# Kernel tuning notes

Hardware: AMD Instinct MI355X
Metric: run time of the kernel (lower is better)

Reference implementation:

```python
import jax, jax.numpy as jnp
import numpy as np

B, N, K = 8, 2048, 20
NC = 50
EPS = 1e-5
SLOPE = 0.2


def _knn(xt, k):
    # xt: [B, N, C]; negative squared euclidean distance, top-k (includes self)
    xx = jnp.sum(xt * xt, axis=-1)                      # [B, N]
    inner = jnp.einsum('bnc,bmc->bnm', xt, xt)          # [B, N, N]
    dist = 2.0 * inner - xx[:, :, None] - xx[:, None, :]
    return jax.lax.top_k(dist, k)[1]                    # [B, N, k] int32


def _edge_conv(xt, w, g, b, k):
    # xt: [B, N, C]; w: [O, 2C]; BatchNorm2d over (B, N, k) per out-channel.
    idx = _knn(xt, k)
    nbr = xt[jnp.arange(B)[:, None, None], idx]          # [B, N, k, C]
    ctr = jnp.broadcast_to(xt[:, :, None, :], nbr.shape)
    edge = jnp.concatenate([nbr - ctr, ctr], axis=-1)    # [B, N, k, 2C]
    h = jnp.einsum('bnkc,oc->bnko', edge, w)             # 1x1 conv, no bias
    mu = jnp.mean(h, axis=(0, 1, 2))
    var = jnp.var(h, axis=(0, 1, 2))
    h = (h - mu) / jnp.sqrt(var + EPS) * g + b
    h = jnp.where(h > 0, h, SLOPE * h)                   # LeakyReLU(0.2)
    return jnp.max(h, axis=2)                            # max over k -> [B, N, O]


def _bn1d(y, g, b):
    mu = jnp.mean(y, axis=0)
    var = jnp.var(y, axis=0)
    return (y - mu) / jnp.sqrt(var + EPS) * g + b


def setup_inputs() -> dict:
    key = jax.random.key(0)
    ks = jax.random.split(key, 20)

    def rn(k, shape, scale):
        return jax.random.normal(k, shape, dtype=jnp.float32) * scale

    d = {
        'x': rn(ks[0], (B * N, 3), 1.0),
        'pos': rn(ks[1], (B * N, 3), 1.0),
        'batch': jnp.repeat(jnp.arange(B, dtype=jnp.int64), N),
        'edge_index': jax.random.randint(ks[2], (2, B * N), 0, B * N, dtype=jnp.int64),
        # EdgeConv 1x1 conv weights [out, in], BN gamma/beta
        'w1': rn(ks[3], (64, 6), 0.3),   'g1': jnp.ones(64),  'b1': jnp.zeros(64),
        'w2': rn(ks[4], (64, 128), 0.1), 'g2': jnp.ones(64),  'b2': jnp.zeros(64),
        'w3': rn(ks[5], (128, 128), 0.1),'g3': jnp.ones(128), 'b3': jnp.zeros(128),
        'w4': rn(ks[6], (256, 256), 0.08),'g4': jnp.ones(256),'b4': jnp.zeros(256),
        # lin1: Linear(512,1024)+ReLU+BN1d(1024)
        'lw1': rn(ks[7], (512, 1024), 0.04), 'lb1': jnp.zeros(1024),
        'lg1': jnp.ones(1024), 'lbb1': jnp.zeros(1024),
        # mlp: [1024->256 +ReLU+BN] -> [256->128 +ReLU+BN] -> Lin(128, NC)
        'mw1': rn(ks[8], (1024, 256), 0.03), 'mb1': jnp.zeros(256),
        'mg1': jnp.ones(256), 'mbb1': jnp.zeros(256),
        'mw2': rn(ks[9], (256, 128), 0.06), 'mb2': jnp.zeros(128),
        'mg2': jnp.ones(128), 'mbb2': jnp.zeros(128),
        'hw': rn(ks[10], (128, NC), 0.09), 'hb': jnp.zeros(NC),
    }
    return d


def reference(x, pos, batch, edge_index,
              w1, g1, b1, w2, g2, b2, w3, g3, b3, w4, g4, b4,
              lw1, lb1, lg1, lbb1,
              mw1, mb1, mg1, mbb1, mw2, mb2, mg2, mbb2,
              hw, hb):
    # batch is sorted with N points per cloud -> static reshape
    xt = x.reshape(B, N, 3)
    x1 = _edge_conv(xt, w1, g1, b1, K)   # [B, N, 64]
    x2 = _edge_conv(x1, w2, g2, b2, K)   # [B, N, 64]
    x3 = _edge_conv(x2, w3, g3, b3, K)   # [B, N, 128]
    x4 = _edge_conv(x3, w4, g4, b4, K)   # [B, N, 256]
    cat = jnp.concatenate([x1, x2, x3, x4], axis=-1)  # [B, N, 512]
    h = cat.reshape(B * N, 512)
    h = _bn1d(jax.nn.relu(h @ lw1 + lb1), lg1, lbb1)
    h = _bn1d(jax.nn.relu(h @ mw1 + mb1), mg1, mbb1)   # dropout = identity (eval)
    h = _bn1d(jax.nn.relu(h @ mw2 + mb2), mg2, mbb2)
    logits = h @ hw + hb
    return jax.nn.log_softmax(logits, axis=1)
```

## Files before the change

### kernel.cpp

```cpp
#include <hip/hip_runtime.h>
#include <math.h>

#define NB 8
#define NP 2048
#define KNBR 20
#define NROWS (NB*NP)
#define SLOPEV 0.2f
#define EPSV 1e-5f

typedef short s8v __attribute__((ext_vector_type(8)));
typedef float f4v __attribute__((ext_vector_type(4)));
typedef double d4v __attribute__((ext_vector_type(4)));

__device__ __forceinline__ unsigned short f2bf(float f) {
    union { float f; unsigned u; } v; v.f = f;
    unsigned r = v.u + 0x7FFFu + ((v.u >> 16) & 1u);
    return (unsigned short)(r >> 16);
}

__global__ void mfma64_probe(int* __restrict__ tab)
{
    const int lane = threadIdx.x;
    d4v z = {0.0, 0.0, 0.0, 0.0};
    d4v pa = __builtin_amdgcn_mfma_f64_16x16x4f64((double)lane, 1.0, z, 0, 0, 0);
    d4v pb = __builtin_amdgcn_mfma_f64_16x16x4f64(1.0, (double)lane, z, 0, 0, 0);
    int famA = 1, famB = 1;
#pragma unroll
    for (int r = 0; r < 4; ++r) {
        int iv = (int)(pa[r] + 0.5);
        int row;
        if ((iv & 3) == 0 && iv >= 96) row = (iv - 96) >> 2;
        else { row = (iv - 6) >> 4; famA = 0; }
        int jv = (int)(pb[r] + 0.5);
        int col;
        if ((jv & 3) == 0 && jv >= 96) col = (jv - 96) >> 2;
        else { col = (jv - 6) >> 4; famB = 0; }
        tab[lane * 8 + r]     = row;
        tab[lane * 8 + 4 + r] = col;
    }
    tab[512 + lane] = famA;
    tab[576 + lane] = famB;
}

template<int KD>
__global__ __launch_bounds__(256, 2) void knn_fused2(
    const double* __restrict__ F, int lda, int C,
    const double* __restrict__ xx,
    double* __restrict__ tmpv, int* __restrict__ tmpc,
    const int* __restrict__ tab)
{
    constexpr int CH = (KD < 16) ? KD : 16;
    __shared__ double Bs[CH][66];
    __shared__ double Tile[64][65];
    __shared__ double thr[64];
    __shared__ unsigned msk[64][2];

    const int tid = threadIdx.x;
    const int wave = tid >> 6, lane = tid & 63;
    const int bb    = blockIdx.z;
    const int half  = blockIdx.y;
    const int r0    = blockIdx.x * 64;
    const int cbase = half * 1024;
    const double* Fb  = F  + (size_t)bb * NP * lda;
    const double* xxb = xx + (size_t)bb * NP;

    int rT[4], cT[4];
#pragma unroll
    for (int r = 0; r < 4; ++r) { rT[r] = tab[lane * 8 + r]; cT[r] = tab[lane * 8 + 4 + r]; }
    const int famA = tab[512];
    const int famB = tab[576];
    const int am = famA ? (lane & 15) : (lane >> 2);
    const int ak = famA ? (lane >> 4) : (lane & 3);
    const int bn = famB ? (lane & 15) : (lane >> 2);
    const int bk = famB ? (lane >> 4) : (lane & 3);

    const int arow = r0 + wave * 16 + am;
    double areg[KD / 4];
#pragma unroll
    for (int j = 0; j < KD / 4; ++j) {
        const int k = j * 4 + ak;
        areg[j] = (k < C) ? Fb[(size_t)arow * lda + k] : 0.0;
    }
    double xr4[4];
#pragma unroll
    for (int rg = 0; rg < 4; ++rg)
        xr4[rg] = xxb[r0 + wave * 16 + rT[rg]];

    double kv[KNBR];
    int    ki[KNBR];
#pragma unroll
    for (int q = 0; q < KNBR; ++q) { kv[q] = -INFINITY; ki[q] = 0; }
    if (tid < 64) { thr[tid] = -INFINITY; msk[tid][0] = 0u; msk[tid][1] = 0u; }
    __syncthreads();

    for (int ct = 0; ct < 16; ++ct) {
        const int c0 = cbase + ct * 64;
        d4v acc[4];
#pragma unroll
        for (int nt = 0; nt < 4; ++nt) acc[nt] = (d4v){0.0, 0.0, 0.0, 0.0};

#pragma unroll
        for (int kc = 0; kc < KD; kc += CH) {
            {
                const int col = tid >> 2;
                const int kb0 = (tid & 3) * (CH / 4);
                const double* bp = Fb + (size_t)(c0 + col) * lda + kc + kb0;
#pragma unroll
                for (int i = 0; i < CH / 4; ++i) {
                    const int k2 = kc + kb0 + i;
                    Bs[kb0 + i][col] = (k2 < C) ? bp[i] : 0.0;
                }
            }
            __syncthreads();
#pragma unroll
            for (int kg = 0; kg < CH / 4; ++kg) {
                const double a  = areg[kc / 4 + kg];
                const double b0 = Bs[kg * 4 + bk][bn];
                const double b1 = Bs[kg * 4 + bk][16 + bn];
                const double b2 = Bs[kg * 4 + bk][32 + bn];
                const double b3 = Bs[kg * 4 + bk][48 + bn];
                acc[0] = __builtin_amdgcn_mfma_f64_16x16x4f64(a, b0, acc[0], 0, 0, 0);
                acc[1] = __builtin_amdgcn_mfma_f64_16x16x4f64(a, b1, acc[1], 0, 0, 0);
                acc[2] = __builtin_amdgcn_mfma_f64_16x16x4f64(a, b2, acc[2], 0, 0, 0);
                acc[3] = __builtin_amdgcn_mfma_f64_16x16x4f64(a, b3, acc[3], 0, 0, 0);
            }
            __syncthreads();
        }

#pragma unroll
        for (int nt = 0; nt < 4; ++nt) {
#pragma unroll
            for (int rg = 0; rg < 4; ++rg) {
                const int rloc = wave * 16 + rT[rg];
                const int cloc = nt * 16 + cT[rg];
                const double d = (2.0 * acc[nt][rg] - xr4[rg]) - xxb[c0 + cloc];
                if (d > thr[rloc]) {
                    Tile[rloc][cloc] = d;
                    atomicOr(&msk[rloc][cloc >> 5], 1u << (cloc & 31));
                }
            }
        }
        __syncthreads();

        if (tid < 64) {
            bool changed = false;
#pragma unroll
            for (int w2 = 0; w2 < 2; ++w2) {
                unsigned m = msk[tid][w2];
                msk[tid][w2] = 0u;
                while (m) {
                    const int b = __ffs(m) - 1;
                    m &= m - 1u;
                    const double v = Tile[tid][w2 * 32 + b];
                    if (v > kv[KNBR - 1]) {
                        const int col = c0 + w2 * 32 + b;
                        int pos = 0;
#pragma unroll
                        for (int q = 0; q < KNBR; ++q) pos += (kv[q] >= v) ? 1 : 0;
#pragma unroll
                        for (int q = KNBR - 1; q >= 0; --q) {
                            if (q > pos)       { kv[q] = kv[q - 1]; ki[q] = ki[q - 1]; }
                            else if (q == pos) { kv[q] = v;         ki[q] = col; }
                        }
                        changed = true;
                    }
                }
            }
            if (changed) thr[tid] = kv[KNBR - 1];
        }
        __syncthreads();
    }

    if (tid < 64) {
        const size_t rowg = (size_t)bb * NP + r0 + tid;
        double* vp = tmpv + (rowg * 2 + half) * KNBR;
        int*    cp = tmpc + (rowg * 2 + half) * KNBR;
#pragma unroll
        for (int q = 0; q < KNBR; ++q) { vp[q] = kv[q]; cp[q] = ki[q]; }
    }
}

__global__ void merge_topk(const double* __restrict__ tmpv,
                           const int* __restrict__ tmpc,
                           int* __restrict__ out)
{
    const int row = blockIdx.x * 256 + threadIdx.x;
    if (row >= NROWS) return;
    const double* va = tmpv + (size_t)row * 2 * KNBR;
    const int*    ca = tmpc + (size_t)row * 2 * KNBR;
    const double* vb = va + KNBR;
    const int*    cb = ca + KNBR;
    const int jbase = (row / NP) * NP;
    int* op = out + (size_t)row * KNBR;
    int ia = 0, ib = 0;
#pragma unroll
    for (int q = 0; q < KNBR; ++q) {
        const double x = va[ia], y = vb[ib];
        const bool takeA = (x > y) || (x == y && ca[ia] < cb[ib]);
        if (takeA) { op[q] = jbase + ca[ia]; ++ia; }
        else       { op[q] = jbase + cb[ib]; ++ib; }
    }
}

#define DK 16
__global__ __launch_bounds__(256, 2) void gemm64(
    const double* __restrict__ A, int lda,
    const double* __restrict__ Bm, int ldb,
    double* __restrict__ P, double* __restrict__ Q, int O, int Kd,
    const int* __restrict__ tab)
{
    __shared__ double As[DK][130];
    __shared__ double Bs[DK][66];
    const int tid = threadIdx.x;
    const int wave = tid >> 6, lane = tid & 63;
    const int quad = lane >> 4, l15 = lane & 15;
    const int row0 = blockIdx.y * 128, col0 = blockIdx.x * 64;

    int rT[4], cT[4];
#pragma unroll
    for (int r = 0; r < 4; ++r) { rT[r] = tab[lane * 8 + r]; cT[r] = tab[lane * 8 + 4 + r]; }
    const int famA = tab[512];
    const int famB = tab[576];
    const int am = famA ? l15 : (lane >> 2);
    const int ak = famA ? quad : (lane & 3);
    const int bn = famB ? l15 : (lane >> 2);
    const int bk = famB ? quad : (lane & 3);

    d4v acc[2][4];
#pragma unroll
    for (int mt = 0; mt < 2; ++mt)
#pragma unroll
        for (int nt = 0; nt < 4; ++nt) acc[mt][nt] = (d4v){0.0, 0.0, 0.0, 0.0};

    const int ma = tid >> 1, ka = (tid & 1) * 8;
    const int mb = tid >> 2, kb = (tid & 3) * 4;

    for (int kc = 0; kc < Kd; kc += DK) {
        const double* ap = A + (size_t)(row0 + ma) * lda + kc + ka;
#pragma unroll
        for (int i = 0; i < 8; ++i) {
            const int k2 = kc + ka + i;
            As[ka + i][ma] = (k2 < Kd) ? ap[i] : 0.0;
        }
        const double* bp = Bm + (size_t)(col0 + mb) * ldb + kc + kb;
#pragma unroll
        for (int i = 0; i < 4; ++i) {
            const int k2 = kc + kb + i;
            Bs[kb + i][mb] = (k2 < Kd) ? bp[i] : 0.0;
        }
        __syncthreads();
#pragma unroll
        for (int kg = 0; kg < 4; ++kg) {
            const int k = kg * 4;
            double a0 = As[k + ak][wave * 32 + am];
            double a1 = As[k + ak][wave * 32 + 16 + am];
            double b0 = Bs[k + bk][bn];
            double b1 = Bs[k + bk][16 + bn];
            double b2 = Bs[k + bk][32 + bn];
            double b3 = Bs[k + bk][48 + bn];
            acc[0][0] = __builtin_amdgcn_mfma_f64_16x16x4f64(a0, b0, acc[0][0], 0, 0, 0);
            acc[0][1] = __builtin_amdgcn_mfma_f64_16x16x4f64(a0, b1, acc[0][1], 0, 0, 0);
            acc[0][2] = __builtin_amdgcn_mfma_f64_16x16x4f64(a0, b2, acc[0][2], 0, 0, 0);
            acc[0][3] = __builtin_amdgcn_mfma_f64_16x16x4f64(a0, b3, acc[0][3], 0, 0, 0);
            acc[1][0] = __builtin_amdgcn_mfma_f64_16x16x4f64(a1, b0, acc[1][0], 0, 0, 0);
            acc[1][1] = __builtin_amdgcn_mfma_f64_16x16x4f64(a1, b1, acc[1][1], 0, 0, 0);
            acc[1][2] = __builtin_amdgcn_mfma_f64_16x16x4f64(a1, b2, acc[1][2], 0, 0, 0);
            acc[1][3] = __builtin_amdgcn_mfma_f64_16x16x4f64(a1, b3, acc[1][3], 0, 0, 0);
        }
        __syncthreads();
    }

    double* dst = (col0 < O) ? P : Q;
    const int cbase = (col0 < O) ? col0 : (col0 - O);
#pragma unroll
    for (int mt = 0; mt < 2; ++mt)
#pragma unroll
        for (int nt = 0; nt < 4; ++nt) {
#pragma unroll
            for (int rg = 0; rg < 4; ++rg) {
                const int r = row0 + wave * 32 + mt * 16 + rT[rg];
                const int c = cbase + nt * 16 + cT[rg];
                dst[(size_t)r * O + c] = acc[mt][nt][rg];
            }
        }
}

__global__ __launch_bounds__(256) void gemm_bf16(
    const float* __restrict__ A, int lda,
    const unsigned short* __restrict__ W,
    float* __restrict__ C, int ldc,
    int Kd,
    const float* __restrict__ bias,
    const float* __restrict__ a_ss)
{
    __shared__ unsigned short As[4][64][8];
    __shared__ unsigned short Bs[4][128][8];
    const int tid = threadIdx.x;
    const int wave = tid >> 6, lane = tid & 63;
    const int quad = lane >> 4, l15 = lane & 15;
    const int row0 = blockIdx.y * 64, col0 = blockIdx.x * 128;

    f4v acc[4][2];
#pragma unroll
    for (int mt = 0; mt < 4; ++mt)
#pragma unroll
        for (int nt = 0; nt < 2; ++nt) acc[mt][nt] = (f4v){0.f, 0.f, 0.f, 0.f};

    const int ar = tid >> 2, akc = tid & 3;
    const int br = tid >> 1, bkc = (tid & 1) * 2;

    for (int kc0 = 0; kc0 < Kd; kc0 += 32) {
        {
            const float* ap = A + (size_t)(row0 + ar) * lda + kc0 + akc * 8;
            float t0[8];
            *(float4*)&t0[0] = *(const float4*)ap;
            *(float4*)&t0[4] = *(const float4*)(ap + 4);
            if (a_ss) {
                const int kb = kc0 + akc * 8;
#pragma unroll
                for (int i = 0; i < 8; ++i)
                    t0[i] = fmaf(t0[i], a_ss[kb + i], a_ss[Kd + kb + i]);
            }
            unsigned short u[8];
#pragma unroll
            for (int i = 0; i < 8; ++i) u[i] = f2bf(t0[i]);
            *(uint4*)&As[akc][ar][0] = *(const uint4*)&u[0];
        }
        {
            const unsigned short* wp = W + (size_t)(col0 + br) * Kd + kc0 + bkc * 8;
            uint4 q0 = *(const uint4*)wp;
            uint4 q1 = *(const uint4*)(wp + 8);
            *(uint4*)&Bs[bkc][br][0]     = q0;
            *(uint4*)&Bs[bkc + 1][br][0] = q1;
        }
        __syncthreads();

        s8v a[4], b[2];
#pragma unroll
        for (int mt = 0; mt < 4; ++mt)
            a[mt] = *(const s8v*)&As[quad][mt * 16 + l15][0];
#pragma unroll
        for (int nt = 0; nt < 2; ++nt)
            b[nt] = *(const s8v*)&Bs[quad][wave * 32 + nt * 16 + l15][0];
#pragma unroll
        for (int mt = 0; mt < 4; ++mt)
#pragma unroll
            for (int nt = 0; nt < 2; ++nt)
                acc[mt][nt] = __builtin_amdgcn_mfma_f32_16x16x32_bf16(
                    a[mt], b[nt], acc[mt][nt], 0, 0, 0);
        __syncthreads();
    }

#pragma unroll
    for (int mt = 0; mt < 4; ++mt)
#pragma unroll
        for (int nt = 0; nt < 2; ++nt) {
            const int col = col0 + wave * 32 + nt * 16 + l15;
            const float bi = bias[col];
#pragma unroll
            for (int r = 0; r < 4; ++r) {
                const int row = row0 + mt * 16 + quad * 4 + r;
                float v = acc[mt][nt][r] + bi;
                v = fmaxf(v, 0.f);
                C[(size_t)row * ldc + col] = v;
            }
        }
}

#define GBK 16
__global__ __launch_bounds__(256, 2) void gemm_f32(
    const float* __restrict__ A, int lda,
    const float* __restrict__ Bm, int ldb,
    float* __restrict__ Cm, int ldc,
    int M, int Nn, int Kd, int mode,
    const float* __restrict__ bias,
    const float* __restrict__ a_ss)
{
    __shared__ float As[GBK][132];
    __shared__ float Bs[GBK][132];
    const int tid = threadIdx.x;
    const int tx = tid & 15, ty = tid >> 4;
    const int lin = blockIdx.y * gridDim.x + blockIdx.x;
    const int bx = lin / gridDim.y;
    const int by = lin - bx * gridDim.y;
    const int row0 = by * 128, col0 = bx * 128;
    float acc[8][8];
#pragma unroll
    for (int i = 0; i < 8; ++i)
#pragma unroll
        for (int j = 0; j < 8; ++j) acc[i][j] = 0.f;

    const int m  = tid >> 1;
    const int kk = (tid & 1) * 8;

    for (int kc = 0; kc < Kd; kc += GBK) {
        const int gc = col0 + m;
        const float* ap = A  + (size_t)(row0 + m) * lda + kc + kk;
        const float* bp = Bm + (size_t)gc * ldb + kc + kk;
#pragma unroll
        for (int i = 0; i < 8; ++i) {
            const int k2 = kc + kk + i;
            float v = 0.f;
            if (k2 < Kd) {
                v = ap[i];
                if (a_ss) v = fmaf(v, a_ss[k2], a_ss[Kd + k2]);
            }
            As[kk + i][m] = v;
        }
#pragma unroll
        for (int i = 0; i < 8; ++i) {
            const int k2 = kc + kk + i;
            float v = 0.f;
            if (gc < Nn && k2 < Kd) v = bp[i];
            Bs[kk + i][m] = v;
        }
        __syncthreads();
#pragma unroll
        for (int k = 0; k < GBK; ++k) {
            float4 a0 = *(const float4*)&As[k][ty * 4];
            float4 a1 = *(const float4*)&As[k][64 + ty * 4];
            float4 b0 = *(const float4*)&Bs[k][tx * 4];
            float4 b1 = *(const float4*)&Bs[k][64 + tx * 4];
            float a[8] = {a0.x, a0.y, a0.z, a0.w, a1.x, a1.y, a1.z, a1.w};
            float b[8] = {b0.x, b0.y, b0.z, b0.w, b1.x, b1.y, b1.z, b1.w};
#pragma unroll
            for (int i = 0; i < 8; ++i)
#pragma unroll
                for (int j = 0; j < 8; ++j) acc[i][j] = fmaf(a[i], b[j], acc[i][j]);
        }
        __syncthreads();
    }

#pragma unroll
    for (int i = 0; i < 8; ++i) {
        const int row = row0 + ty * 4 + (i & 3) + ((i >> 2) << 6);
        if (row >= M) continue;
#pragma unroll
        for (int h = 0; h < 2; ++h) {
            const int c0 = col0 + tx * 4 + (h << 6);
#pragma unroll
            for (int j = 0; j < 4; ++j) {
                const int col = c0 + j;
                if (col < Nn) {
                    float t = acc[i][h * 4 + j];
                    if (mode == 2)      t = fmaxf(t + bias[col], 0.f);
                    else if (mode == 3) t = t + bias[col];
                    Cm[(size_t)row * ldc + col] = t;
                }
            }
        }
    }
}

__global__ void f2d_kernel(const float* __restrict__ in, double* __restrict__ out, long n)
{
    long t = (long)blockIdx.x * 256 + threadIdx.x;
    if (t < n) out[t] = (double)in[t];
}
__global__ void d2f_kernel(const double* __restrict__ in, float* __restrict__ out, long n)
{
    long t = (long)blockIdx.x * 256 + threadIdx.x;
    if (t < n) out[t] = (float)in[t];
}

__global__ void xx_kernel_d(const double* __restrict__ F, int lda, int C,
                            double* __restrict__ xx)
{
    int r = blockIdx.x * 256 + threadIdx.x;
    if (r >= NROWS) return;
    const double* p = F + (long)r * lda;
    double s = 0.0;
    for (int c = 0; c < C; ++c) { double v = p[c]; s = fma(v, v, s); }
    xx[r] = s;
}

__global__ void wmod_kernel_d(const float* __restrict__ w, double* __restrict__ wm,
                              int O, int C)
{
    int t = blockIdx.x * 256 + threadIdx.x;
    if (t >= O * C) return;
    int o = t / C, c = t - o * C;
    double a = (double)w[o * 2 * C + c];
    double b = (double)w[o * 2 * C + C + c];
    wm[o * C + c] = a;
    wm[(O + o) * C + c] = b - a;
}

__global__ void transpose_kernel(const float* __restrict__ in, float* __restrict__ out,
                                 int R, int C)
{
    long t = (long)blockIdx.x * 256 + threadIdx.x;
    if (t >= (long)R * C) return;
    int r = (int)(t / C), c = (int)(t - (long)r * C);
    out[(long)c * R + r] = in[t];
}

__global__ void transpose_bf(const float* __restrict__ in, unsigned short* __restrict__ out,
                             int R, int C)
{
    long t = (long)blockIdx.x * 256 + threadIdx.x;
    if (t >= (long)R * C) return;
    int r = (int)(t / C), c = (int)(t - (long)r * C);
    out[(long)c * R + r] = f2bf(in[t]);
}

__global__ __launch_bounds__(256) void edge_gather(const double* __restrict__ P,
                                                   const double* __restrict__ Q,
                                                   const int* __restrict__ idx,
                                                   int O, int shiftO,
                                                   double* __restrict__ sums,
                                                   double* __restrict__ catOut, int ldo)
{
    const int tid = threadIdx.x;
    const int o = tid & (O - 1);
    const int q = tid >> shiftO;
    const int nsub = 256 >> shiftO;
    const int lin = blockIdx.x;
    const int r0 = (lin & 7) * NP + (lin >> 3) * 16;
    double s = 0.0, ss = 0.0;
    for (int r = r0 + q; r < r0 + 16; r += nsub) {
        const double qv = Q[(size_t)r * O + o];
        const int* ip = idx + r * KNBR;
        double m = -INFINITY;
        for (int k = 0; k < KNBR; ++k) {
            const int j = ip[k];
            const double v = P[(size_t)j * O + o] + qv;
            s += v; ss = fma(v, v, ss);
            m = fmax(m, v);
        }
        catOut[(size_t)r * ldo + o] = m;
    }
    __shared__ double red[256];
    red[tid] = s; __syncthreads();
    if (q == 0) for (int qq = 1; qq < nsub; ++qq) s += red[o + (qq << shiftO)];
    __syncthreads();
    red[tid] = ss; __syncthreads();
    if (q == 0) {
        for (int qq = 1; qq < nsub; ++qq) ss += red[o + (qq << shiftO)];
        atomicAdd(&sums[o], s);
        atomicAdd(&sums[O + o], ss);
    }
}

__global__ void bn_finalize_d(const double* __restrict__ sums,
                              const float* __restrict__ g, const float* __restrict__ b,
                              double* __restrict__ ss, int O, double invCnt)
{
    int o = blockIdx.x * 256 + threadIdx.x;
    if (o >= O) return;
    double mu  = sums[o] * invCnt;
    double var = sums[O + o] * invCnt - mu * mu;
    double is  = 1.0 / sqrt(var + 1e-5);
    double sc  = (double)g[o] * is;
    ss[o] = sc;
    ss[O + o] = (double)b[o] - mu * sc;
}

__global__ __launch_bounds__(256) void bn_apply(double* __restrict__ catOut, int ldo,
                                                const double* __restrict__ ssb,
                                                int O, int shiftO,
                                                const double* __restrict__ P,
                                                const double* __restrict__ Q,
                                                const int* __restrict__ idx)
{
    const int t = blockIdx.x * 256 + threadIdx.x;
    const int o = t & (O - 1);
    const int r = t >> shiftO;
    const double sc = ssb[o], sh = ssb[O + o];
    double v = catOut[(size_t)r * ldo + o];
    if (sc < 0.0) {
        const double qv = Q[(size_t)r * O + o];
        const int* ip = idx + r * KNBR;
        double m = INFINITY;
        for (int k = 0; k < KNBR; ++k)
            m = fmin(m, P[(size_t)ip[k] * O + o] + qv);
        v = m;
    }
    double u = fma(v, sc, sh);
    u = u > 0.0 ? u : 0.2 * u;
    catOut[(size_t)r * ldo + o] = u;
}

__global__ void col_stats(const float* __restrict__ Y, int ncol,
                          float* __restrict__ sums)
{
    int c  = blockIdx.x * 128 + threadIdx.x;
    int r0 = blockIdx.y * 256;
    float s = 0.f, ss = 0.f;
    for (int r = r0; r < r0 + 256; ++r) {
        float v = Y[(long)r * ncol + c];
        s += v; ss = fmaf(v, v, ss);
    }
    atomicAdd(&sums[c], s);
    atomicAdd(&sums[ncol + c], ss);
}

__global__ void bn_finalize_f(const float* __restrict__ sums,
                              const float* __restrict__ g, const float* __restrict__ b,
                              float* __restrict__ ss, int O, float invCnt)
{
    int o = blockIdx.x * 256 + threadIdx.x;
    if (o >= O) return;
    float mu  = sums[o] * invCnt;
    float var = sums[O + o] * invCnt - mu * mu;
    float is  = rsqrtf(var + EPSV);
    float sc  = g[o] * is;
    ss[o] = sc;
    ss[O + o] = b[o] - mu * sc;
}

__global__ __launch_bounds__(256) void log_softmax_kernel(float* __restrict__ Y)
{
    const int lane = threadIdx.x & 63;
    const int row  = blockIdx.x * 4 + (threadIdx.x >> 6);
    float v = -INFINITY;
    if (lane < 50) v = Y[(long)row * 50 + lane];
    float mx = v;
#pragma unroll
    for (int off = 32; off >= 1; off >>= 1) mx = fmaxf(mx, __shfl_xor(mx, off, 64));
    float e = (lane < 50) ? expf(v - mx) : 0.f;
    float s = e;
#pragma unroll
    for (int off = 32; off >= 1; off >>= 1) s += __shfl_xor(s, off, 64);
    float l = logf(s) + mx;
    if (lane < 50) Y[(long)row * 50 + lane] = v - l;
}

extern "C" void kernel_launch(void* const* d_in, const int* in_sizes, int n_in,
                              void* d_out, int out_size, void* d_ws, size_t ws_size,
                              hipStream_t stream)
{
    const float* x   = (const float*)d_in[0];
    const float* w[4]  = {(const float*)d_in[4], (const float*)d_in[7],
                          (const float*)d_in[10], (const float*)d_in[13]};
    const float* g[4]  = {(const float*)d_in[5], (const float*)d_in[8],
                          (const float*)d_in[11], (const float*)d_in[14]};
    const float* bb[4] = {(const float*)d_in[6], (const float*)d_in[9],
                          (const float*)d_in[12], (const float*)d_in[15]};
    const float* lw1 = (const float*)d_in[16]; const float* lb1 = (const float*)d_in[17];
    const float* lg1 = (const float*)d_in[18]; const float* lbb1 = (const float*)d_in[19];
    const float* mw1 = (const float*)d_in[20]; const float* mb1 = (const float*)d_in[21];
    const float* mg1 = (const float*)d_in[22]; const float* mbb1 = (const float*)d_in[23];
    const float* mw2 = (const float*)d_in[24]; const float* mb2 = (const float*)d_in[25];
    const float* mg2 = (const float*)d_in[26]; const float* mbb2 = (const float*)d_in[27];
    const float* hw  = (const float*)d_in[28]; const float* hb  = (const float*)d_in[29];
    float* out = (float*)d_out;

    char* base = (char*)d_ws;
    double* catD = (double*)base;
    char*  un    = base + 67108864;
    double* tmpv = (double*)un;
    int*    tmpc = (int*)(un + 5242880);
    double* Pb   = (double*)un;
    double* Qb   = (double*)(un + 33554432);
    float* cat32 = (float*)un;
    float* Y2    = (float*)(un + 33554432);
    float* Y3    = (float*)(un + 50331648);
    unsigned short* lw1Tb = (unsigned short*)(un + 58720256);
    unsigned short* mw1Tb = (unsigned short*)(un + 59768832);
    unsigned short* mw2Tb = (unsigned short*)(un + 60293120);
    float* hwT   = (float*)(un + 60358656);
    float* Y1    = (float*)base;
    char* tail = base + 2u * 67108864u;
    int*    idxb  = (int*)tail;
    double* xD    = (double*)(tail + 1310720);
    double* xxD   = (double*)(tail + 1703936);
    double* wmodD = (double*)(tail + 1835008);
    double* sumsD = (double*)(tail + 2359296);
    double* ssbD  = (double*)(tail + 2367488);
    float*  sumsF = (float*)(tail + 2375680);
    float*  ssbF  = (float*)(tail + 2383872);
    int*    mtab  = (int*)(tail + 2392064);

    mfma64_probe<<<1, 64, 0, stream>>>(mtab);

    f2d_kernel<<<(NROWS * 3 + 255) / 256, 256, 0, stream>>>(x, xD, (long)NROWS * 3);

    const double* Fin[4] = {xD, catD + 0, catD + 64, catD + 128};
    const int   ldaL[4] = {3, 512, 512, 512};
    const int   CL[4]   = {3, 64, 64, 128};
    const int   OL[4]   = {64, 64, 128, 256};
    const int   coff[4] = {0, 64, 128, 256};

    for (int l = 0; l < 4; ++l) {
        const double* F = Fin[l];
        const int lda = ldaL[l], C = CL[l], O = OL[l];
        const int shiftO = (O == 64) ? 6 : (O == 128) ? 7 : 8;

        wmod_kernel_d<<<(O * C + 255) / 256, 256, 0, stream>>>(w[l], wmodD, O, C);
        xx_kernel_d<<<NROWS / 256, 256, 0, stream>>>(F, lda, C, xxD);

        dim3 kg(NP / 64, 2, NB);
        if (C == 3)
            knn_fused2<4><<<kg, 256, 0, stream>>>(F, lda, C, xxD, tmpv, tmpc, mtab);
        else if (C == 64)
            knn_fused2<64><<<kg, 256, 0, stream>>>(F, lda, C, xxD, tmpv, tmpc, mtab);
        else
            knn_fused2<128><<<kg, 256, 0, stream>>>(F, lda, C, xxD, tmpv, tmpc, mtab);
        merge_topk<<<NROWS / 256, 256, 0, stream>>>(tmpv, tmpc, idxb);

        gemm64<<<dim3((2 * O) / 64, NROWS / 128), 256, 0, stream>>>(
            F, lda, wmodD, C, Pb, Qb, O, C, mtab);

        hipMemsetAsync(sumsD, 0, 2 * O * sizeof(double), stream);
        edge_gather<<<NROWS / 16, 256, 0, stream>>>(Pb, Qb, idxb, O, shiftO, sumsD,
                                                    catD + coff[l], 512);
        bn_finalize_d<<<(O + 255) / 256, 256, 0, stream>>>(sumsD, g[l], bb[l], ssbD, O,
                                                           1.0 / ((double)NROWS * KNBR));
        bn_apply<<<(NROWS * O) / 256, 256, 0, stream>>>(catD + coff[l], 512, ssbD,
                                                        O, shiftO, Pb, Qb, idxb);
    }

    d2f_kernel<<<((long)NROWS * 512 + 255) / 256, 256, 0, stream>>>(catD, cat32, (long)NROWS * 512);

    transpose_bf<<<(512 * 1024 + 255) / 256, 256, 0, stream>>>(lw1, lw1Tb, 512, 1024);
    transpose_bf<<<(1024 * 256 + 255) / 256, 256, 0, stream>>>(mw1, mw1Tb, 1024, 256);
    transpose_bf<<<(256 * 128 + 255) / 256, 256, 0, stream>>>(mw2, mw2Tb, 256, 128);
    transpose_kernel<<<(128 * 50 + 255) / 256, 256, 0, stream>>>(hw, hwT, 128, 50);

    {
        gemm_bf16<<<dim3(1024 / 128, NROWS / 64), 256, 0, stream>>>(
            cat32, 512, lw1Tb, Y1, 1024, 512, lb1, nullptr);
        hipMemsetAsync(sumsF, 0, 2 * 1024 * sizeof(float), stream);
        col_stats<<<dim3(1024 / 128, 64), 128, 0, stream>>>(Y1, 1024, sumsF);
        bn_finalize_f<<<4, 256, 0, stream>>>(sumsF, lg1, lbb1, ssbF, 1024, 1.f / NROWS);
    }
    {
        gemm_bf16<<<dim3(256 / 128, NROWS / 64), 256, 0, stream>>>(
            Y1, 1024, mw1Tb, Y2, 256, 1024, mb1, ssbF);
        hipMemsetAsync(sumsF, 0, 2 * 256 * sizeof(float), stream);
        col_stats<<<dim3(256 / 128, 64), 128, 0, stream>>>(Y2, 256, sumsF);
        bn_finalize_f<<<1, 256, 0, stream>>>(sumsF, mg1, mbb1, ssbF, 256, 1.f / NROWS);
    }
    {
        gemm_bf16<<<dim3(128 / 128, NROWS / 64), 256, 0, stream>>>(
            Y2, 256, mw2Tb, Y3, 128, 256, mb2, ssbF);
        hipMemsetAsync(sumsF, 0, 2 * 128 * sizeof(float), stream);
        col_stats<<<dim3(1, 64), 128, 0, stream>>>(Y3, 128, sumsF);
        bn_finalize_f<<<1, 256, 0, stream>>>(sumsF, mg2, mbb2, ssbF, 128, 1.f / NROWS);
    }
    {
        dim3 gg(1, NROWS / 128);
        gemm_f32<<<gg, 256, 0, stream>>>(Y3, 128, hwT, 128, out, 50,
                                         NROWS, 50, 128, 3, hb, ssbF);
        log_softmax_kernel<<<NROWS / 4, 256, 0, stream>>>(out);
    }
}
```

Baseline: 1.932 ms.

## Load kNN B operands directly from global memory and remap block order by batch

The kNN distance GEMM no longer stages column features through a shared-memory tile with two barriers per k-chunk. Each lane now loads its MFMA B operands straight from global memory, relying on cache reuse across waves. Block indices are also remapped so that consecutive blocks interleave batches, which may spread work and improve L2 locality. The trade-off is uncoalesced strided global loads (row stride lda doubles) in place of coalesced shared-memory staging, in exchange for fewer syncs and less shared memory.

```diff
diff --git a/kernel.cpp b/kernel.cpp
--- a/kernel.cpp
+++ b/kernel.cpp
@@ -43,23 +43,23 @@
 }
 
 template<int KD>
-__global__ __launch_bounds__(256, 2) void knn_fused2(
+__global__ __launch_bounds__(256, 2) void knn_fused3(
     const double* __restrict__ F, int lda, int C,
     const double* __restrict__ xx,
     double* __restrict__ tmpv, int* __restrict__ tmpc,
     const int* __restrict__ tab)
 {
-    constexpr int CH = (KD < 16) ? KD : 16;
-    __shared__ double Bs[CH][66];
     __shared__ double Tile[64][65];
     __shared__ double thr[64];
     __shared__ unsigned msk[64][2];
 
     const int tid = threadIdx.x;
     const int wave = tid >> 6, lane = tid & 63;
-    const int bb    = blockIdx.z;
-    const int half  = blockIdx.y;
-    const int r0    = blockIdx.x * 64;
+    const int lin  = (blockIdx.z * gridDim.y + blockIdx.y) * gridDim.x + blockIdx.x;
+    const int bb   = lin & 7;
+    const int rest = lin >> 3;
+    const int half = rest >> 5;
+    const int r0   = (rest & 31) * 64;
     const int cbase = half * 1024;
     const double* Fb  = F  + (size_t)bb * NP * lda;
     const double* xxb = xx + (size_t)bb * NP;
@@ -99,32 +99,29 @@
 #pragma unroll
         for (int nt = 0; nt < 4; ++nt) acc[nt] = (d4v){0.0, 0.0, 0.0, 0.0};
 
-#pragma unroll
-        for (int kc = 0; kc < KD; kc += CH) {
-            {
-                const int col = tid >> 2;
-                const int kb0 = (tid & 3) * (CH / 4);
-                const double* bp = Fb + (size_t)(c0 + col) * lda + kc + kb0;
-#pragma unroll
-                for (int i = 0; i < CH / 4; ++i) {
-                    const int k2 = kc + kb0 + i;
-                    Bs[kb0 + i][col] = (k2 < C) ? bp[i] : 0.0;
-                }
+        const double* bp0 = Fb + (size_t)(c0      + bn) * lda;
+        const double* bp1 = Fb + (size_t)(c0 + 16 + bn) * lda;
+        const double* bp2 = Fb + (size_t)(c0 + 32 + bn) * lda;
+        const double* bp3 = Fb + (size_t)(c0 + 48 + bn) * lda;
+
+#pragma unroll 4
+        for (int kg = 0; kg < KD / 4; ++kg) {
+            const int k = kg * 4 + bk;
+            double b0, b1, b2, b3;
+            if (KD == 4) {
+                const bool gok = (k < C);
+                b0 = gok ? bp0[k] : 0.0;
+                b1 = gok ? bp1[k] : 0.0;
+                b2 = gok ? bp2[k] : 0.0;
+                b3 = gok ? bp3[k] : 0.0;
+            } else {
+                b0 = bp0[k]; b1 = bp1[k]; b2 = bp2[k]; b3 = bp3[k];
             }
-            __syncthreads();
-#pragma unroll
-            for (int kg = 0; kg < CH / 4; ++kg) {
-                const double a  = areg[kc / 4 + kg];
-                const double b0 = Bs[kg * 4 + bk][bn];
-                const double b1 = Bs[kg * 4 + bk][16 + bn];
-                const double b2 = Bs[kg * 4 + bk][32 + bn];
-                const double b3 = Bs[kg * 4 + bk][48 + bn];
-                acc[0] = __builtin_amdgcn_mfma_f64_16x16x4f64(a, b0, acc[0], 0, 0, 0);
-                acc[1] = __builtin_amdgcn_mfma_f64_16x16x4f64(a, b1, acc[1], 0, 0, 0);
-                acc[2] = __builtin_amdgcn_mfma_f64_16x16x4f64(a, b2, acc[2], 0, 0, 0);
-                acc[3] = __builtin_amdgcn_mfma_f64_16x16x4f64(a, b3, acc[3], 0, 0, 0);
-            }
-            __syncthreads();
+            const double a = areg[kg];
+            acc[0] = __builtin_amdgcn_mfma_f64_16x16x4f64(a, b0, acc[0], 0, 0, 0);
+            acc[1] = __builtin_amdgcn_mfma_f64_16x16x4f64(a, b1, acc[1], 0, 0, 0);
+            acc[2] = __builtin_amdgcn_mfma_f64_16x16x4f64(a, b2, acc[2], 0, 0, 0);
+            acc[3] = __builtin_amdgcn_mfma_f64_16x16x4f64(a, b3, acc[3], 0, 0, 0);
         }
 
 #pragma unroll
@@ -692,11 +689,11 @@
 
         dim3 kg(NP / 64, 2, NB);
         if (C == 3)
-            knn_fused2<4><<<kg, 256, 0, stream>>>(F, lda, C, xxD, tmpv, tmpc, mtab);
+            knn_fused3<4><<<kg, 256, 0, stream>>>(F, lda, C, xxD, tmpv, tmpc, mtab);
         else if (C == 64)
-            knn_fused2<64><<<kg, 256, 0, stream>>>(F, lda, C, xxD, tmpv, tmpc, mtab);
+            knn_fused3<64><<<kg, 256, 0, stream>>>(F, lda, C, xxD, tmpv, tmpc, mtab);
         else
-            knn_fused2<128><<<kg, 256, 0, stream>>>(F, lda, C, xxD, tmpv, tmpc, mtab);
+            knn_fused3<128><<<kg, 256, 0, stream>>>(F, lda, C, xxD, tmpv, tmpc, mtab);
         merge_topk<<<NROWS / 256, 256, 0, stream>>>(tmpv, tmpc, idxb);
 
         gemm64<<<dim3((2 * O) / 64, NROWS / 128), 256, 0, stream>>>(
```

Result: slower. 2.501 ms (+29.5%).
